# Performance work log

Measured on AMD Instinct MI355X. Metric: run time of the kernel, lower is better.

The kernel has to match this reference:

```python
import jax, jax.numpy as jnp
import numpy as np
from jax import lax

# geomloss SamplesLoss('sinkhorn', p=2, blur=0.01, scaling=0.9) semantics:
# debiased Sinkhorn divergence S_eps(a,b) = OT_eps(x,y) - 0.5*OT_eps(x,x) - 0.5*OT_eps(y,y)
# with cost C = ||x-y||^2 / 2, uniform weights, and epsilon annealing from
# diameter^p down to blur^p with ratio scaling^p.
P = 2
BLUR = 0.01
SCALING = 0.9
DIAMETER = 8.0  # static upper bound on point-cloud spread for randn data

def _eps_schedule():
    scales = []
    s = DIAMETER
    while s > BLUR:
        scales.append(s)
        s *= SCALING
    scales.append(BLUR)
    return jnp.asarray(np.array(scales, np.float32) ** P)

def _sqcost(x, y):
    # x: [B,N,D], y: [B,M,D] -> C[B,N,M] = 0.5*||x_i-y_j||^2
    x2 = jnp.sum(x * x, -1)[:, :, None]
    y2 = jnp.sum(y * y, -1)[:, None, :]
    return 0.5 * (x2 + y2 - 2.0 * jnp.einsum('bnd,bmd->bnm', x, y))

def _sinkhorn_divergence(x, y):
    B, N, _ = x.shape
    M = y.shape[1]
    logN = jnp.log(jnp.float32(N))
    logM = jnp.log(jnp.float32(M))
    eps_list = _eps_schedule()

    Cxy = _sqcost(x, y)          # [B,N,M]
    Cyx = jnp.swapaxes(Cxy, 1, 2)
    Cxx = _sqcost(x, x)
    Cyy = _sqcost(y, y)

    def softmin(eps, C, h, logw):
        # -eps * log sum_j exp(log w_j + (h_j - C_ij)/eps)
        return -eps * jax.nn.logsumexp((h[:, None, :] - C) / eps - logw, axis=-1)

    # potentials computed under envelope theorem (no grad through iterations)
    Cxy_d, Cyx_d = lax.stop_gradient(Cxy), lax.stop_gradient(Cyx)
    Cxx_d, Cyy_d = lax.stop_gradient(Cxx), lax.stop_gradient(Cyy)

    z = jnp.zeros((B, N), x.dtype)
    zy = jnp.zeros((B, M), x.dtype)

    def body(carry, eps):
        f, g, fx, gy = carry
        ft = softmin(eps, Cxy_d, g, logM)
        gt = softmin(eps, Cyx_d, f, logN)
        f, g = 0.5 * (f + ft), 0.5 * (g + gt)
        fx = 0.5 * (fx + softmin(eps, Cxx_d, fx, logN))
        gy = 0.5 * (gy + softmin(eps, Cyy_d, gy, logM))
        return (f, g, fx, gy), None

    (f, g, fx, gy), _ = lax.scan(body, (z, zy, z, zy), eps_list)

    # last extrapolation at target eps, differentiable w.r.t. the costs
    eps_t = eps_list[-1]
    f_fin = softmin(eps_t, Cxy, lax.stop_gradient(g), logM)
    g_fin = softmin(eps_t, Cyx, lax.stop_gradient(f), logN)
    fx_fin = softmin(eps_t, Cxx, lax.stop_gradient(fx), logN)
    gy_fin = softmin(eps_t, Cyy, lax.stop_gradient(gy), logM)

    # S = <a, f - fx> + <b, g - gy>, uniform weights
    return jnp.mean(f_fin - fx_fin, axis=-1) + jnp.mean(g_fin - gy_fin, axis=-1)  # [B]


def setup_inputs() -> dict:
    key = jax.random.key(0)
    k1, k2 = jax.random.split(key)
    B, N, D = 8, 2048, 3
    p1 = jax.random.normal(k1, (B, N, D), dtype=jnp.float32)
    p2 = jax.random.normal(k2, (B, N, D), dtype=jnp.float32)
    return {"p1": p1, "p2": p2}


def reference(p1, p2):
    # EMD_Loss.forward: mean over batch of per-sample Sinkhorn divergences
    return jnp.mean(_sinkhorn_divergence(p1, p2))
```

## Files before the change

### kernel.cpp

```cpp
#include <hip/hip_runtime.h>
#include <math.h>

#define NPTS 2048
#define NB 8
#define R 2
#define NW 16
#define BROWS 128
#define CPAIR 64

typedef float v2f __attribute__((ext_vector_type(2)));

__device__ __forceinline__ float wexp2(float v) { return __builtin_amdgcn_exp2f(v); }
__device__ __forceinline__ v2f fma2(v2f a, v2f b, v2f c) {
  return __builtin_elementwise_fma(a, b, c);
}
__device__ __forceinline__ v2f max2(v2f a, v2f b) {
  return __builtin_elementwise_max(a, b);
}

__global__ __launch_bounds__(256) void emd_init(const float* __restrict__ x,
                                                const float* __restrict__ y,
                                                float4* __restrict__ x4,
                                                float4* __restrict__ y4,
                                                float* __restrict__ pot0,
                                                float* __restrict__ out) {
  int t = blockIdx.x * blockDim.x + threadIdx.x;
  if (t < NB * NPTS) {
    float a0 = x[3 * t], a1 = x[3 * t + 1], a2 = x[3 * t + 2];
    x4[t] = make_float4(a0, a1, a2, 0.5f * (a0 * a0 + a1 * a1 + a2 * a2));
    float b0 = y[3 * t], b1 = y[3 * t + 1], b2 = y[3 * t + 2];
    y4[t] = make_float4(b0, b1, b2, 0.5f * (b0 * b0 + b1 * b1 + b2 * b2));
  }
  pot0[t] = 0.0f;
  if (t == 0) out[0] = 0.0f;
}


__global__ __launch_bounds__(1024, 8) void emd_sweep_boot(
    const float4* __restrict__ x4, const float4* __restrict__ y4,
    const float* __restrict__ pot_in, float* __restrict__ pot_out,
    float* __restrict__ amax_out, float c, float neg_eps_ln2, float eps_logM) {
  __shared__ union {
    struct {
      float4 A[NPTS / 2];
      float4 B[NPTS / 2];
    } cp;
    struct {
      float m[NW][BROWS];
      float l[NW][BROWS];
    } mg;
  } sh;

  int blk = blockIdx.x;
  int mat = blk >> 7;
  int b = (blk >> 4) & 7;
  int rg = blk & 15;
  int tid = threadIdx.x;
  int lane = tid & 63;
  int w = tid >> 6;

  const float4* rowp = (mat == 1 || mat == 3) ? y4 : x4;
  const float4* colp = (mat == 0 || mat == 3) ? y4 : x4;
  int hidx = (mat < 2) ? (mat ^ 1) : mat;
  const float* h = pot_in + (hidx * NB + b) * NPTS;
  const float4* colb = colp + b * NPTS;

  {
    float4 q0 = colb[2 * tid];
    float4 q1 = colb[2 * tid + 1];
    float2 hv = ((const float2*)h)[tid];
    sh.cp.A[tid] = make_float4(q0.x, q1.x, q0.y, q1.y);
    sh.cp.B[tid] = make_float4(q0.z, q1.z, (hv.x - q0.w) * c, (hv.y - q1.w) * c);
  }
  __syncthreads();

  int rowbase = rg * BROWS;
  const float4* rowb = rowp + b * NPTS + rowbase;

  v2f xs0[R], xs1[R], xs2[R];
  float m[R], l[R];
#pragma unroll
  for (int r = 0; r < R; ++r) {
    float4 p = rowb[r * 64 + lane];
    float a0 = p.x * c, a1 = p.y * c, a2 = p.z * c;
    xs0[r] = (v2f){a0, a0};
    xs1[r] = (v2f){a1, a1};
    xs2[r] = (v2f){a2, a2};
    m[r] = -INFINITY;
    l[r] = 0.0f;
  }

  int p0 = w * CPAIR;
  for (int tp = 0; tp < CPAIR; tp += 4) {
    float4 A[4], B[4];
#pragma unroll
    for (int j = 0; j < 4; ++j) {
      A[j] = sh.cp.A[p0 + tp + j];
      B[j] = sh.cp.B[p0 + tp + j];
    }
#pragma unroll
    for (int r = 0; r < R; ++r) {
      v2f s2[4];
#pragma unroll
      for (int j = 0; j < 4; ++j) {
        v2f qx = {A[j].x, A[j].y};
        v2f qy = {A[j].z, A[j].w};
        v2f qz = {B[j].x, B[j].y};
        v2f qw = {B[j].z, B[j].w};
        s2[j] = fma2(xs0[r], qx, fma2(xs1[r], qy, fma2(xs2[r], qz, qw)));
      }
      v2f t0 = max2(s2[0], s2[1]);
      v2f t1 = max2(s2[2], s2[3]);
      v2f u = max2(t0, t1);
      float mt = fmaxf(u.x, u.y);
      float mn = fmaxf(m[r], mt);
      v2f mn2 = {mn, mn};
      v2f acc = {0.0f, 0.0f};
#pragma unroll
      for (int j = 0; j < 4; ++j) {
        v2f d = s2[j] - mn2;
        v2f e;
        e.x = wexp2(d.x);
        e.y = wexp2(d.y);
        acc += e;
      }
      float er = wexp2(m[r] - mn);
      l[r] = fmaf(l[r], er, acc.x + acc.y);
      m[r] = mn;
    }
  }

  __syncthreads();
#pragma unroll
  for (int r = 0; r < R; ++r) {
    sh.mg.m[w][r * 64 + lane] = m[r];
    sh.mg.l[w][r * 64 + lane] = l[r];
  }
  __syncthreads();

  if (w < 2) {
    int row = w * 64 + lane;
    float M = sh.mg.m[0][row];
#pragma unroll
    for (int q = 1; q < NW; ++q) M = fmaxf(M, sh.mg.m[q][row]);
    float L = 0.0f;
#pragma unroll
    for (int q = 0; q < NW; ++q)
      L += sh.mg.l[q][row] * wexp2(sh.mg.m[q][row] - M);
    float pw = rowb[row].w;
    float res = pw + neg_eps_ln2 * (M + log2f(L)) + eps_logM;
    float invc = -neg_eps_ln2;
    amax_out[(mat * NB + b) * NPTS + rowbase + row] = M * invc;
    const float* oldp = pot_in + (mat * NB + b) * NPTS + rowbase;
    float* outp = pot_out + (mat * NB + b) * NPTS + rowbase;
    outp[row] = 0.5f * (oldp[row] + res);
  }
}

template <bool FINAL>
__global__ __launch_bounds__(1024, 8) void emd_sweep_ref(
    const float4* __restrict__ x4, const float4* __restrict__ y4,
    const float* __restrict__ pot_in, float* __restrict__ pot_out,
    const float* __restrict__ amax_in, float* __restrict__ amax_out,
    float* __restrict__ out, float c, float neg_eps_ln2, float eps_logM) {
  __shared__ union {
    struct {
      float4 A[NPTS / 2];
      float4 B[NPTS / 2];
    } cp;
    float lbuf[NW][BROWS];
  } sh;

  int blk = blockIdx.x;
  int mat = blk >> 7;
  int b = (blk >> 4) & 7;
  int rg = blk & 15;
  int tid = threadIdx.x;
  int lane = tid & 63;
  int w = tid >> 6;

  const float4* rowp = (mat == 1 || mat == 3) ? y4 : x4;
  const float4* colp = (mat == 0 || mat == 3) ? y4 : x4;
  int hidx = (mat < 2) ? (mat ^ 1) : mat;
  const float* h = pot_in + (hidx * NB + b) * NPTS;
  const float4* colb = colp + b * NPTS;

  {
    float4 q0 = colb[2 * tid];
    float4 q1 = colb[2 * tid + 1];
    float2 hv = ((const float2*)h)[tid];
    sh.cp.A[tid] = make_float4(q0.x, q1.x, q0.y, q1.y);
    sh.cp.B[tid] = make_float4(q0.z, q1.z, (hv.x - q0.w) * c, (hv.y - q1.w) * c);
  }

  int rowbase = rg * BROWS;
  const float4* rowb = rowp + b * NPTS + rowbase;
  const float* amrow = amax_in + (mat * NB + b) * NPTS + rowbase;

  v2f xs0[R], xs1[R], xs2[R], mref2[R], acc[R];
#pragma unroll
  for (int r = 0; r < R; ++r) {
    float4 p = rowb[r * 64 + lane];
    float a0 = p.x * c, a1 = p.y * c, a2 = p.z * c;
    xs0[r] = (v2f){a0, a0};
    xs1[r] = (v2f){a1, a1};
    xs2[r] = (v2f){a2, a2};
    float mr = amrow[r * 64 + lane] * c;
    mref2[r] = (v2f){mr, mr};
    acc[r] = (v2f){0.0f, 0.0f};
  }
  __syncthreads();

  int p0 = w * CPAIR;
  for (int tp = 0; tp < CPAIR; tp += 4) {
    float4 A[4], B[4];
#pragma unroll
    for (int j = 0; j < 4; ++j) {
      A[j] = sh.cp.A[p0 + tp + j];
      B[j] = sh.cp.B[p0 + tp + j];
    }
#pragma unroll
    for (int r = 0; r < R; ++r) {
#pragma unroll
      for (int j = 0; j < 4; ++j) {
        v2f qx = {A[j].x, A[j].y};
        v2f qy = {A[j].z, A[j].w};
        v2f qz = {B[j].x, B[j].y};
        v2f qw = {B[j].z, B[j].w};
        v2f s2 = fma2(xs0[r], qx, fma2(xs1[r], qy, fma2(xs2[r], qz, qw)));
        v2f d = s2 - mref2[r];
        v2f e;
        e.x = wexp2(d.x);
        e.y = wexp2(d.y);
        acc[r] += e;
      }
    }
  }

  __syncthreads();
#pragma unroll
  for (int r = 0; r < R; ++r)
    sh.lbuf[w][r * 64 + lane] = acc[r].x + acc[r].y;
  __syncthreads();

  if (w < 2) {
    int row = w * 64 + lane;
    float L = sh.lbuf[0][row];
#pragma unroll
    for (int q = 1; q < NW; ++q) L += sh.lbuf[q][row];
    float mr = amrow[row] * c;
    float lse = mr + log2f(L);
    float pw = rowb[row].w;
    float res = pw + neg_eps_ln2 * lse + eps_logM;
    float invc = -neg_eps_ln2;
    if (FINAL) {
      float sign = (mat < 2) ? 1.0f : -1.0f;
      float val = sign * res * (1.0f / (float)(NB * NPTS));
#pragma unroll
      for (int off = 32; off; off >>= 1) val += __shfl_xor(val, off);
      if (lane == 0) atomicAdd(out, val);
    } else {
      amax_out[(mat * NB + b) * NPTS + rowbase + row] = lse * invc;
      const float* oldp = pot_in + (mat * NB + b) * NPTS + rowbase;
      float* outp = pot_out + (mat * NB + b) * NPTS + rowbase;
      outp[row] = 0.5f * (oldp[row] + res);
    }
  }
}

extern "C" void kernel_launch(void* const* d_in, const int* in_sizes, int n_in,
                              void* d_out, int out_size, void* d_ws, size_t ws_size,
                              hipStream_t stream) {
  const float* x = (const float*)d_in[0];
  const float* y = (const float*)d_in[1];
  float* out = (float*)d_out;

  char* ws = (char*)d_ws;
  float4* x4 = (float4*)ws;
  float4* y4 = (float4*)(ws + 262144);
  float* pot = (float*)(ws + 524288);
  float* amax = (float*)(ws + 1048576);

  emd_init<<<256, 256, 0, stream>>>(x, y, x4, y4, pot, out);

  float eps_arr[80];
  int ne = 0;
  double s = 8.0;
  while (s > 0.01) {
    float sf = (float)s;
    eps_arr[ne++] = sf * sf;
    s *= 0.9;
  }
  {
    float bf = 0.01f;
    eps_arr[ne++] = bf * bf;
  }

  const double LOG2E = 1.4426950408889634;
  const double LN2 = 0.6931471805599453;
  const double LOG2048 = 7.624618986159398;

  int cur = 0;
  for (int k = 0; k < ne; ++k) {
    float eps = eps_arr[k];
    float c = (float)(LOG2E / (double)eps);
    float nel = (float)(-(double)eps * LN2);
    float elM = (float)((double)eps * LOG2048);
    if (k == 0) {
      emd_sweep_boot<<<512, 1024, 0, stream>>>(x4, y4, pot + cur * 65536,
                                               pot + (1 - cur) * 65536, amax,
                                               c, nel, elM);
    } else {
      emd_sweep_ref<false><<<512, 1024, 0, stream>>>(
          x4, y4, pot + cur * 65536, pot + (1 - cur) * 65536, amax, amax, out,
          c, nel, elM);
    }
    cur ^= 1;
  }

  {
    float eps = eps_arr[ne - 1];
    float c = (float)(LOG2E / (double)eps);
    float nel = (float)(-(double)eps * LN2);
    float elM = (float)((double)eps * LOG2048);
    emd_sweep_ref<true><<<512, 1024, 0, stream>>>(
        x4, y4, pot + cur * 65536, nullptr, amax, nullptr, out, c, nel, elM);
  }
}
```

Baseline: 1.378 ms.

## Prepack column data in global memory and stream it via scalar loads

The previous sweep writes the next iteration's scaled potential term directly into a prepacked column buffer, laid out in the pair-interleaved format. The refine kernel then reads column data with wave-uniform s_load_dwordx8 scalar loads instead of staging it through LDS. This removes the per-block LDS fill, one barrier, and the per-column LDS reads. The costs are a scalar-load wait on every 4-pair chunk, since there is no software prefetch, and extra global writes and workspace for two packed buffers.

```diff
diff --git a/kernel.cpp b/kernel.cpp
--- a/kernel.cpp
+++ b/kernel.cpp
@@ -8,7 +8,10 @@
 #define BROWS 128
 #define CPAIR 64
 
+#define CPK_FLOATS 8192
+
 typedef float v2f __attribute__((ext_vector_type(2)));
+typedef float v8f __attribute__((ext_vector_type(8)));
 
 __device__ __forceinline__ float wexp2(float v) { return __builtin_amdgcn_exp2f(v); }
 __device__ __forceinline__ v2f fma2(v2f a, v2f b, v2f c) {
@@ -23,6 +26,8 @@
                                                 float4* __restrict__ x4,
                                                 float4* __restrict__ y4,
                                                 float* __restrict__ pot0,
+                                                float* __restrict__ cpk0,
+                                                float* __restrict__ cpk1,
                                                 float* __restrict__ out) {
   int t = blockIdx.x * blockDim.x + threadIdx.x;
   if (t < NB * NPTS) {
@@ -32,6 +37,23 @@
     y4[t] = make_float4(b0, b1, b2, 0.5f * (b0 * b0 + b1 * b1 + b2 * b2));
   }
   pot0[t] = 0.0f;
+  {
+    int mat = t >> 14;
+    int b = (t >> 11) & 7;
+    int col = t & 2047;
+    const float* src = (mat == 1 || mat == 2) ? x : y;
+    int si = (b * NPTS + col) * 3;
+    float qx = src[si], qy = src[si + 1], qz = src[si + 2];
+    int p = col >> 1, par = col & 1;
+    int g = p >> 2, sl = p & 3;
+    int base = (mat * NB + b) * CPK_FLOATS + g * 32;
+    cpk0[base + sl * 4 + par] = qx;
+    cpk0[base + sl * 4 + 2 + par] = qy;
+    cpk0[base + 16 + sl * 4 + par] = qz;
+    cpk1[base + sl * 4 + par] = qx;
+    cpk1[base + sl * 4 + 2 + par] = qy;
+    cpk1[base + 16 + sl * 4 + par] = qz;
+  }
   if (t == 0) out[0] = 0.0f;
 }
 
@@ -39,7 +61,8 @@
 __global__ __launch_bounds__(1024, 8) void emd_sweep_boot(
     const float4* __restrict__ x4, const float4* __restrict__ y4,
     const float* __restrict__ pot_in, float* __restrict__ pot_out,
-    float* __restrict__ amax_out, float c, float neg_eps_ln2, float eps_logM) {
+    float* __restrict__ amax_out, float* __restrict__ cpk_out, float c,
+    float neg_eps_ln2, float eps_logM, float cnext) {
   __shared__ union {
     struct {
       float4 A[NPTS / 2];
@@ -153,7 +176,13 @@
     amax_out[(mat * NB + b) * NPTS + rowbase + row] = M * invc;
     const float* oldp = pot_in + (mat * NB + b) * NPTS + rowbase;
     float* outp = pot_out + (mat * NB + b) * NPTS + rowbase;
-    outp[row] = 0.5f * (oldp[row] + res);
+    float np = 0.5f * (oldp[row] + res);
+    outp[row] = np;
+    int mp = (mat < 2) ? (mat ^ 1) : mat;
+    int col = rowbase + row;
+    int p = col >> 1, par = col & 1, g = p >> 2, sl = p & 3;
+    cpk_out[(mp * NB + b) * CPK_FLOATS + g * 32 + 16 + sl * 4 + 2 + par] =
+        (np - pw) * cnext;
   }
 }
 
@@ -162,14 +191,10 @@
     const float4* __restrict__ x4, const float4* __restrict__ y4,
     const float* __restrict__ pot_in, float* __restrict__ pot_out,
     const float* __restrict__ amax_in, float* __restrict__ amax_out,
-    float* __restrict__ out, float c, float neg_eps_ln2, float eps_logM) {
-  __shared__ union {
-    struct {
-      float4 A[NPTS / 2];
-      float4 B[NPTS / 2];
-    } cp;
-    float lbuf[NW][BROWS];
-  } sh;
+    const float* __restrict__ cpk_in, float* __restrict__ cpk_out,
+    float* __restrict__ out, float c, float neg_eps_ln2, float eps_logM,
+    float cnext) {
+  __shared__ float lbuf[NW][BROWS];
 
   int blk = blockIdx.x;
   int mat = blk >> 7;
@@ -180,18 +205,6 @@
   int w = tid >> 6;
 
   const float4* rowp = (mat == 1 || mat == 3) ? y4 : x4;
-  const float4* colp = (mat == 0 || mat == 3) ? y4 : x4;
-  int hidx = (mat < 2) ? (mat ^ 1) : mat;
-  const float* h = pot_in + (hidx * NB + b) * NPTS;
-  const float4* colb = colp + b * NPTS;
-
-  {
-    float4 q0 = colb[2 * tid];
-    float4 q1 = colb[2 * tid + 1];
-    float2 hv = ((const float2*)h)[tid];
-    sh.cp.A[tid] = make_float4(q0.x, q1.x, q0.y, q1.y);
-    sh.cp.B[tid] = make_float4(q0.z, q1.z, (hv.x - q0.w) * c, (hv.y - q1.w) * c);
-  }
 
   int rowbase = rg * BROWS;
   const float4* rowb = rowp + b * NPTS + rowbase;
@@ -209,24 +222,34 @@
     mref2[r] = (v2f){mr, mr};
     acc[r] = (v2f){0.0f, 0.0f};
   }
-  __syncthreads();
-
-  int p0 = w * CPAIR;
-  for (int tp = 0; tp < CPAIR; tp += 4) {
-    float4 A[4], B[4];
+
+  int wu = __builtin_amdgcn_readfirstlane(w);
+  unsigned long long cp0 =
+      (unsigned long long)(cpk_in + (mat * NB + b) * CPK_FLOATS) +
+      (unsigned long long)(wu * 2048);
+
+  for (int it = 0; it < 16; ++it) {
+    unsigned long long addr = cp0 + (unsigned)(it * 128);
+    v8f a0, a1, b0, b1;
+    asm volatile(
+        "s_load_dwordx8 %0, %4, 0x0\n\t"
+        "s_load_dwordx8 %1, %4, 0x20\n\t"
+        "s_load_dwordx8 %2, %4, 0x40\n\t"
+        "s_load_dwordx8 %3, %4, 0x60\n\t"
+        "s_waitcnt lgkmcnt(0)"
+        : "=s"(a0), "=s"(a1), "=s"(b0), "=s"(b1)
+        : "s"(addr));
 #pragma unroll
     for (int j = 0; j < 4; ++j) {
-      A[j] = sh.cp.A[p0 + tp + j];
-      B[j] = sh.cp.B[p0 + tp + j];
-    }
-#pragma unroll
-    for (int r = 0; r < R; ++r) {
-#pragma unroll
-      for (int j = 0; j < 4; ++j) {
-        v2f qx = {A[j].x, A[j].y};
-        v2f qy = {A[j].z, A[j].w};
-        v2f qz = {B[j].x, B[j].y};
-        v2f qw = {B[j].z, B[j].w};
+      v8f va = (j < 2) ? a0 : a1;
+      v8f vb = (j < 2) ? b0 : b1;
+      int o = (j & 1) * 4;
+      v2f qx = {va[o], va[o + 1]};
+      v2f qy = {va[o + 2], va[o + 3]};
+      v2f qz = {vb[o], vb[o + 1]};
+      v2f qw = {vb[o + 2], vb[o + 3]};
+#pragma unroll
+      for (int r = 0; r < R; ++r) {
         v2f s2 = fma2(xs0[r], qx, fma2(xs1[r], qy, fma2(xs2[r], qz, qw)));
         v2f d = s2 - mref2[r];
         v2f e;
@@ -237,17 +260,16 @@
     }
   }
 
-  __syncthreads();
 #pragma unroll
   for (int r = 0; r < R; ++r)
-    sh.lbuf[w][r * 64 + lane] = acc[r].x + acc[r].y;
+    lbuf[w][r * 64 + lane] = acc[r].x + acc[r].y;
   __syncthreads();
 
   if (w < 2) {
     int row = w * 64 + lane;
-    float L = sh.lbuf[0][row];
-#pragma unroll
-    for (int q = 1; q < NW; ++q) L += sh.lbuf[q][row];
+    float L = lbuf[0][row];
+#pragma unroll
+    for (int q = 1; q < NW; ++q) L += lbuf[q][row];
     float mr = amrow[row] * c;
     float lse = mr + log2f(L);
     float pw = rowb[row].w;
@@ -263,7 +285,13 @@
       amax_out[(mat * NB + b) * NPTS + rowbase + row] = lse * invc;
       const float* oldp = pot_in + (mat * NB + b) * NPTS + rowbase;
       float* outp = pot_out + (mat * NB + b) * NPTS + rowbase;
-      outp[row] = 0.5f * (oldp[row] + res);
+      float np = 0.5f * (oldp[row] + res);
+      outp[row] = np;
+      int mp = (mat < 2) ? (mat ^ 1) : mat;
+      int col = rowbase + row;
+      int p = col >> 1, par = col & 1, g = p >> 2, sl = p & 3;
+      cpk_out[(mp * NB + b) * CPK_FLOATS + g * 32 + 16 + sl * 4 + 2 + par] =
+          (np - pw) * cnext;
     }
   }
 }
@@ -280,8 +308,10 @@
   float4* y4 = (float4*)(ws + 262144);
   float* pot = (float*)(ws + 524288);
   float* amax = (float*)(ws + 1048576);
-
-  emd_init<<<256, 256, 0, stream>>>(x, y, x4, y4, pot, out);
+  float* cpk[2] = {(float*)(ws + 1310720),
+                   (float*)(ws + 2359296)};
+
+  emd_init<<<256, 256, 0, stream>>>(x, y, x4, y4, pot, cpk[0], cpk[1], out);
 
   float eps_arr[80];
   int ne = 0;
@@ -300,30 +330,35 @@
   const double LN2 = 0.6931471805599453;
   const double LOG2048 = 7.624618986159398;
 
+  float c_arr[80];
+  for (int k = 0; k < ne; ++k) c_arr[k] = (float)(LOG2E / (double)eps_arr[k]);
+
   int cur = 0;
   for (int k = 0; k < ne; ++k) {
     float eps = eps_arr[k];
-    float c = (float)(LOG2E / (double)eps);
+    float ck = c_arr[k];
     float nel = (float)(-(double)eps * LN2);
     float elM = (float)((double)eps * LOG2048);
+    float cn = (k + 1 < ne) ? c_arr[k + 1] : c_arr[ne - 1];
     if (k == 0) {
-      emd_sweep_boot<<<512, 1024, 0, stream>>>(x4, y4, pot + cur * 65536,
-                                               pot + (1 - cur) * 65536, amax,
-                                               c, nel, elM);
+      emd_sweep_boot<<<512, 1024, 0, stream>>>(
+          x4, y4, pot + cur * 65536, pot + (1 - cur) * 65536, amax,
+          cpk[1 - cur], ck, nel, elM, cn);
     } else {
       emd_sweep_ref<false><<<512, 1024, 0, stream>>>(
-          x4, y4, pot + cur * 65536, pot + (1 - cur) * 65536, amax, amax, out,
-          c, nel, elM);
+          x4, y4, pot + cur * 65536, pot + (1 - cur) * 65536, amax, amax,
+          cpk[cur], cpk[1 - cur], out, ck, nel, elM, cn);
     }
     cur ^= 1;
   }
 
   {
     float eps = eps_arr[ne - 1];
-    float c = (float)(LOG2E / (double)eps);
+    float ck = c_arr[ne - 1];
     float nel = (float)(-(double)eps * LN2);
     float elM = (float)((double)eps * LOG2048);
     emd_sweep_ref<true><<<512, 1024, 0, stream>>>(
-        x4, y4, pot + cur * 65536, nullptr, amax, nullptr, out, c, nel, elM);
-  }
-}
+        x4, y4, pot + cur * 65536, nullptr, amax, nullptr, cpk[cur], nullptr,
+        out, ck, nel, elM, 0.0f);
+  }
+}
```

Measured after the change: 1.531 ms. 11.1% more time.

## Morton-sort point clouds and skip column tiles via bounding-box softmin bounds

Applied to the files above, without the earlier changes.

Adds a preprocessing kernel that sorts each cloud by a 3D Morton code, plus a kernel that computes per-tile and per-row-group bounding boxes. In the refinement sweeps, each block uses these boxes, the max potential per tile and the min reference max to bound every tile's contribution, and skips column tiles whose exp2 terms fall below 2^-64. Work is then spread over warps round-robin across the surviving tiles. The aim is to cut exp work at small eps, at the cost of load imbalance across warps, a ballot and extra syncs, and an approximation error bounded by the threshold.

```diff
diff --git a/kernel.cpp b/kernel.cpp
--- a/kernel.cpp
+++ b/kernel.cpp
@@ -6,9 +6,12 @@
 #define R 2
 #define NW 16
 #define BROWS 128
-#define CPAIR 64
+#define NTILE 64
+#define TPAIR 16
+#define NRG 16
 
 typedef float v2f __attribute__((ext_vector_type(2)));
+typedef unsigned long long ull;
 
 __device__ __forceinline__ float wexp2(float v) { return __builtin_amdgcn_exp2f(v); }
 __device__ __forceinline__ v2f fma2(v2f a, v2f b, v2f c) {
@@ -18,37 +21,112 @@
   return __builtin_elementwise_max(a, b);
 }
 
-__global__ __launch_bounds__(256) void emd_init(const float* __restrict__ x,
-                                                const float* __restrict__ y,
-                                                float4* __restrict__ x4,
-                                                float4* __restrict__ y4,
-                                                float* __restrict__ pot0,
-                                                float* __restrict__ out) {
-  int t = blockIdx.x * blockDim.x + threadIdx.x;
-  if (t < NB * NPTS) {
-    float a0 = x[3 * t], a1 = x[3 * t + 1], a2 = x[3 * t + 2];
-    x4[t] = make_float4(a0, a1, a2, 0.5f * (a0 * a0 + a1 * a1 + a2 * a2));
-    float b0 = y[3 * t], b1 = y[3 * t + 1], b2 = y[3 * t + 2];
-    y4[t] = make_float4(b0, b1, b2, 0.5f * (b0 * b0 + b1 * b1 + b2 * b2));
-  }
-  pot0[t] = 0.0f;
-  if (t == 0) out[0] = 0.0f;
-}
-
+__device__ __forceinline__ unsigned quantc(float v) {
+  float u = (v + 6.0f) * (127.0f / 12.0f);
+  int q = (int)u;
+  q = q < 0 ? 0 : (q > 127 ? 127 : q);
+  return (unsigned)q;
+}
+__device__ __forceinline__ unsigned spread3(unsigned v) {
+  unsigned r = 0;
+#pragma unroll
+  for (int i = 0; i < 7; ++i) r |= ((v >> i) & 1u) << (3 * i);
+  return r;
+}
+
+__global__ __launch_bounds__(1024) void emd_sort(const float* __restrict__ x,
+                                                 const float* __restrict__ y,
+                                                 float4* __restrict__ x4s,
+                                                 float4* __restrict__ y4s,
+                                                 float* __restrict__ pot0,
+                                                 float* __restrict__ out) {
+  __shared__ unsigned keys[NPTS];
+  int blk = blockIdx.x;
+  int cloud = blk >> 3, b = blk & 7;
+  const float* src = cloud ? y : x;
+  float4* dst = cloud ? y4s : x4s;
+  int tid = threadIdx.x;
+
+  for (int i = tid; i < NPTS; i += 1024) {
+    int si = (b * NPTS + i) * 3;
+    unsigned qx = quantc(src[si]), qy = quantc(src[si + 1]), qz = quantc(src[si + 2]);
+    unsigned m = spread3(qx) | (spread3(qy) << 1) | (spread3(qz) << 2);
+    keys[i] = (m << 11) | (unsigned)i;
+  }
+  __syncthreads();
+  for (int k = 2; k <= NPTS; k <<= 1) {
+    for (int j = k >> 1; j > 0; j >>= 1) {
+      for (int i = tid; i < NPTS; i += 1024) {
+        int ixj = i ^ j;
+        if (ixj > i) {
+          unsigned a = keys[i], c2 = keys[ixj];
+          bool up = ((i & k) == 0);
+          if ((a > c2) == up) { keys[i] = c2; keys[ixj] = a; }
+        }
+      }
+      __syncthreads();
+    }
+  }
+  for (int p = tid; p < NPTS; p += 1024) {
+    int id = keys[p] & 2047;
+    int si = (b * NPTS + id) * 3;
+    float a0 = src[si], a1 = src[si + 1], a2 = src[si + 2];
+    dst[b * NPTS + p] = make_float4(a0, a1, a2, 0.5f * (a0 * a0 + a1 * a1 + a2 * a2));
+  }
+  int gt = blk * 1024 + tid;
+  for (int i = gt; i < 2 * NB * NPTS; i += 16 * 1024) {
+    pot0[i] = 0.0f;
+    pot0[NB * NPTS * 2 + i] = 0.0f;
+  }
+  if (gt == 0) out[0] = 0.0f;
+}
+
+__global__ __launch_bounds__(256) void emd_meta(const float4* __restrict__ x4s,
+                                                const float4* __restrict__ y4s,
+                                                float* __restrict__ tilebb,
+                                                float* __restrict__ rgbb) {
+  int blk = blockIdx.x;
+  int cloud = blk >> 3, b = blk & 7;
+  const float4* base = (cloud ? y4s : x4s) + b * NPTS;
+  int t = threadIdx.x;
+  float lo0 = 1e30f, lo1 = 1e30f, lo2 = 1e30f;
+  float hi0 = -1e30f, hi1 = -1e30f, hi2 = -1e30f;
+#pragma unroll
+  for (int i = 0; i < 8; ++i) {
+    float4 p = base[t * 8 + i];
+    lo0 = fminf(lo0, p.x); hi0 = fmaxf(hi0, p.x);
+    lo1 = fminf(lo1, p.y); hi1 = fmaxf(hi1, p.y);
+    lo2 = fminf(lo2, p.z); hi2 = fmaxf(hi2, p.z);
+  }
+#pragma unroll
+  for (int off = 2; off; off >>= 1) {
+    lo0 = fminf(lo0, __shfl_xor(lo0, off)); hi0 = fmaxf(hi0, __shfl_xor(hi0, off));
+    lo1 = fminf(lo1, __shfl_xor(lo1, off)); hi1 = fmaxf(hi1, __shfl_xor(hi1, off));
+    lo2 = fminf(lo2, __shfl_xor(lo2, off)); hi2 = fmaxf(hi2, __shfl_xor(hi2, off));
+  }
+  if ((t & 3) == 0) {
+    float* o = tilebb + (blk * NTILE + (t >> 2)) * 8;
+    o[0] = lo0; o[1] = lo1; o[2] = lo2; o[3] = hi0; o[4] = hi1; o[5] = hi2;
+  }
+#pragma unroll
+  for (int off = 8; off >= 4; off >>= 1) {
+    lo0 = fminf(lo0, __shfl_xor(lo0, off)); hi0 = fmaxf(hi0, __shfl_xor(hi0, off));
+    lo1 = fminf(lo1, __shfl_xor(lo1, off)); hi1 = fmaxf(hi1, __shfl_xor(hi1, off));
+    lo2 = fminf(lo2, __shfl_xor(lo2, off)); hi2 = fmaxf(hi2, __shfl_xor(hi2, off));
+  }
+  if ((t & 15) == 0) {
+    float* o = rgbb + (blk * NRG + (t >> 4)) * 8;
+    o[0] = lo0; o[1] = lo1; o[2] = lo2; o[3] = hi0; o[4] = hi1; o[5] = hi2;
+  }
+}
 
 __global__ __launch_bounds__(1024, 8) void emd_sweep_boot(
-    const float4* __restrict__ x4, const float4* __restrict__ y4,
+    const float4* __restrict__ x4s, const float4* __restrict__ y4s,
     const float* __restrict__ pot_in, float* __restrict__ pot_out,
     float* __restrict__ amax_out, float c, float neg_eps_ln2, float eps_logM) {
   __shared__ union {
-    struct {
-      float4 A[NPTS / 2];
-      float4 B[NPTS / 2];
-    } cp;
-    struct {
-      float m[NW][BROWS];
-      float l[NW][BROWS];
-    } mg;
+    struct { float4 A[NPTS / 2]; float4 B[NPTS / 2]; } cp;
+    struct { float m[NW][BROWS]; float l[NW][BROWS]; } mg;
   } sh;
 
   int blk = blockIdx.x;
@@ -59,8 +137,8 @@
   int lane = tid & 63;
   int w = tid >> 6;
 
-  const float4* rowp = (mat == 1 || mat == 3) ? y4 : x4;
-  const float4* colp = (mat == 0 || mat == 3) ? y4 : x4;
+  const float4* rowp = (mat == 1 || mat == 3) ? y4s : x4s;
+  const float4* colp = (mat == 0 || mat == 3) ? y4s : x4s;
   int hidx = (mat < 2) ? (mat ^ 1) : mat;
   const float* h = pot_in + (hidx * NB + b) * NPTS;
   const float4* colb = colp + b * NPTS;
@@ -90,8 +168,8 @@
     l[r] = 0.0f;
   }
 
-  int p0 = w * CPAIR;
-  for (int tp = 0; tp < CPAIR; tp += 4) {
+  int p0 = w * 64;
+  for (int tp = 0; tp < 64; tp += 4) {
     float4 A[4], B[4];
 #pragma unroll
     for (int j = 0; j < 4; ++j) {
@@ -159,17 +237,18 @@
 
 template <bool FINAL>
 __global__ __launch_bounds__(1024, 8) void emd_sweep_ref(
-    const float4* __restrict__ x4, const float4* __restrict__ y4,
+    const float4* __restrict__ x4s, const float4* __restrict__ y4s,
     const float* __restrict__ pot_in, float* __restrict__ pot_out,
     const float* __restrict__ amax_in, float* __restrict__ amax_out,
+    const float* __restrict__ tilebb, const float* __restrict__ rgbb,
     float* __restrict__ out, float c, float neg_eps_ln2, float eps_logM) {
   __shared__ union {
-    struct {
-      float4 A[NPTS / 2];
-      float4 B[NPTS / 2];
-    } cp;
+    struct { float4 A[NPTS / 2]; float4 B[NPTS / 2]; } cp;
     float lbuf[NW][BROWS];
   } sh;
+  __shared__ float Wt[NTILE];
+  __shared__ float wmin[NW];
+  __shared__ ull smask;
 
   int blk = blockIdx.x;
   int mat = blk >> 7;
@@ -179,8 +258,10 @@
   int lane = tid & 63;
   int w = tid >> 6;
 
-  const float4* rowp = (mat == 1 || mat == 3) ? y4 : x4;
-  const float4* colp = (mat == 0 || mat == 3) ? y4 : x4;
+  int cr = (mat == 1 || mat == 3) ? 1 : 0;
+  int cc = (mat == 0 || mat == 3) ? 1 : 0;
+  const float4* rowp = cr ? y4s : x4s;
+  const float4* colp = cc ? y4s : x4s;
   int hidx = (mat < 2) ? (mat ^ 1) : mat;
   const float* h = pot_in + (hidx * NB + b) * NPTS;
   const float4* colb = colp + b * NPTS;
@@ -189,8 +270,13 @@
     float4 q0 = colb[2 * tid];
     float4 q1 = colb[2 * tid + 1];
     float2 hv = ((const float2*)h)[tid];
+    float qwx = (hv.x - q0.w) * c, qwy = (hv.y - q1.w) * c;
     sh.cp.A[tid] = make_float4(q0.x, q1.x, q0.y, q1.y);
-    sh.cp.B[tid] = make_float4(q0.z, q1.z, (hv.x - q0.w) * c, (hv.y - q1.w) * c);
+    sh.cp.B[tid] = make_float4(q0.z, q1.z, qwx, qwy);
+    float wq = fmaxf(qwx, qwy);
+#pragma unroll
+    for (int off = 8; off; off >>= 1) wq = fmaxf(wq, __shfl_xor(wq, off));
+    if ((tid & 15) == 0) Wt[tid >> 4] = wq;
   }
 
   int rowbase = rg * BROWS;
@@ -198,6 +284,7 @@
   const float* amrow = amax_in + (mat * NB + b) * NPTS + rowbase;
 
   v2f xs0[R], xs1[R], xs2[R], mref2[R], acc[R];
+  float amn = 1e30f;
 #pragma unroll
   for (int r = 0; r < R; ++r) {
     float4 p = rowb[r * 64 + lane];
@@ -205,34 +292,65 @@
     xs0[r] = (v2f){a0, a0};
     xs1[r] = (v2f){a1, a1};
     xs2[r] = (v2f){a2, a2};
-    float mr = amrow[r * 64 + lane] * c;
+    float am = amrow[r * 64 + lane];
+    amn = fminf(amn, am);
+    float mr = am * c;
     mref2[r] = (v2f){mr, mr};
     acc[r] = (v2f){0.0f, 0.0f};
   }
-  __syncthreads();
-
-  int p0 = w * CPAIR;
-  for (int tp = 0; tp < CPAIR; tp += 4) {
-    float4 A[4], B[4];
-#pragma unroll
-    for (int j = 0; j < 4; ++j) {
-      A[j] = sh.cp.A[p0 + tp + j];
-      B[j] = sh.cp.B[p0 + tp + j];
-    }
-#pragma unroll
-    for (int r = 0; r < R; ++r) {
+#pragma unroll
+  for (int off = 32; off; off >>= 1) amn = fminf(amn, __shfl_xor(amn, off));
+  if (lane == 0) wmin[w] = amn;
+  __syncthreads();
+
+  if (w == 0) {
+    float a2 = wmin[0];
+#pragma unroll
+    for (int q = 1; q < NW; ++q) a2 = fminf(a2, wmin[q]);
+    const float* rb = rgbb + ((cr * NB + b) * NRG + rg) * 8;
+    float rl0 = rb[0], rl1 = rb[1], rl2 = rb[2];
+    float rh0 = rb[3], rh1 = rb[4], rh2 = rb[5];
+    const float* tb = tilebb + ((cc * NB + b) * NTILE + lane) * 8;
+    float t0 = tb[0], t1 = tb[1], t2 = tb[2], t3 = tb[3], t4 = tb[4], t5 = tb[5];
+    float dm = fmaxf(fmaxf(rl0 * t0, rl0 * t3), fmaxf(rh0 * t0, rh0 * t3)) +
+               fmaxf(fmaxf(rl1 * t1, rl1 * t4), fmaxf(rh1 * t1, rh1 * t4)) +
+               fmaxf(fmaxf(rl2 * t2, rl2 * t5), fmaxf(rh2 * t2, rh2 * t5));
+    float bound = fmaf(c, dm, Wt[lane]) - a2 * c;
+    ull bal = __ballot(bound >= -64.0f);
+    if (lane == 0) smask = bal;
+  }
+  __syncthreads();
+  ull mask = smask;
+
+  int ord = 0;
+  for (int t = 0; t < NTILE; ++t) {
+    if (!((mask >> t) & 1)) continue;
+    if ((ord++ & 15) != w) continue;
+    int pb = t * TPAIR;
+#pragma unroll
+    for (int ii = 0; ii < 4; ++ii) {
+      int p0 = pb + ii * 4;
+      float4 A[4], B[4];
 #pragma unroll
       for (int j = 0; j < 4; ++j) {
-        v2f qx = {A[j].x, A[j].y};
-        v2f qy = {A[j].z, A[j].w};
-        v2f qz = {B[j].x, B[j].y};
-        v2f qw = {B[j].z, B[j].w};
-        v2f s2 = fma2(xs0[r], qx, fma2(xs1[r], qy, fma2(xs2[r], qz, qw)));
-        v2f d = s2 - mref2[r];
-        v2f e;
-        e.x = wexp2(d.x);
-        e.y = wexp2(d.y);
-        acc[r] += e;
+        A[j] = sh.cp.A[p0 + j];
+        B[j] = sh.cp.B[p0 + j];
+      }
+#pragma unroll
+      for (int r = 0; r < R; ++r) {
+#pragma unroll
+        for (int j = 0; j < 4; ++j) {
+          v2f qx = {A[j].x, A[j].y};
+          v2f qy = {A[j].z, A[j].w};
+          v2f qz = {B[j].x, B[j].y};
+          v2f qw = {B[j].z, B[j].w};
+          v2f s2 = fma2(xs0[r], qx, fma2(xs1[r], qy, fma2(xs2[r], qz, qw)));
+          v2f d = s2 - mref2[r];
+          v2f e;
+          e.x = wexp2(d.x);
+          e.y = wexp2(d.y);
+          acc[r] += e;
+        }
       }
     }
   }
@@ -276,12 +394,15 @@
   float* out = (float*)d_out;
 
   char* ws = (char*)d_ws;
-  float4* x4 = (float4*)ws;
-  float4* y4 = (float4*)(ws + 262144);
+  float4* x4s = (float4*)ws;
+  float4* y4s = (float4*)(ws + 262144);
   float* pot = (float*)(ws + 524288);
   float* amax = (float*)(ws + 1048576);
-
-  emd_init<<<256, 256, 0, stream>>>(x, y, x4, y4, pot, out);
+  float* tilebb = (float*)(ws + 1310720);
+  float* rgbb = (float*)(ws + 1343488);
+
+  emd_sort<<<16, 1024, 0, stream>>>(x, y, x4s, y4s, pot, out);
+  emd_meta<<<16, 256, 0, stream>>>(x4s, y4s, tilebb, rgbb);
 
   float eps_arr[80];
   int ne = 0;
@@ -307,13 +428,13 @@
     float nel = (float)(-(double)eps * LN2);
     float elM = (float)((double)eps * LOG2048);
     if (k == 0) {
-      emd_sweep_boot<<<512, 1024, 0, stream>>>(x4, y4, pot + cur * 65536,
+      emd_sweep_boot<<<512, 1024, 0, stream>>>(x4s, y4s, pot + cur * 65536,
                                                pot + (1 - cur) * 65536, amax,
                                                c, nel, elM);
     } else {
       emd_sweep_ref<false><<<512, 1024, 0, stream>>>(
-          x4, y4, pot + cur * 65536, pot + (1 - cur) * 65536, amax, amax, out,
-          c, nel, elM);
+          x4s, y4s, pot + cur * 65536, pot + (1 - cur) * 65536, amax, amax,
+          tilebb, rgbb, out, c, nel, elM);
     }
     cur ^= 1;
   }
@@ -324,6 +445,7 @@
     float nel = (float)(-(double)eps * LN2);
     float elM = (float)((double)eps * LOG2048);
     emd_sweep_ref<true><<<512, 1024, 0, stream>>>(
-        x4, y4, pot + cur * 65536, nullptr, amax, nullptr, out, c, nel, elM);
-  }
-}
+        x4s, y4s, pot + cur * 65536, nullptr, amax, nullptr, tilebb, rgbb,
+        out, c, nel, elM);
+  }
+}
```

Result: slower. 1.839 ms (+33.4%).
